# Performance work log

Measured on AMD Instinct MI355X. Metric: run time of the kernel, lower is better.

## Reference

```python
import jax, jax.numpy as jnp
import numpy as np

N = 12288
D = 128
NUM_BATCH = 32
EPS = 1e-8


def setup_inputs() -> dict:
    key = jax.random.key(0)
    kq, kk, kv, kb = jax.random.split(key, 4)
    Q = jax.random.normal(kq, (N, D), dtype=jnp.float32)
    K = jax.random.normal(kk, (N, D), dtype=jnp.float32)
    V = jax.random.normal(kv, (N, D), dtype=jnp.float32)
    batch_seg = jnp.sort(jax.random.randint(kb, (N,), 0, NUM_BATCH, dtype=jnp.int32))
    return {"Q": Q, "K": K, "V": V, "num_batch": NUM_BATCH, "batch_seg": batch_seg}


def reference(Q, K, V, num_batch, batch_seg):
    d = Q.shape[-1]
    dot = Q @ K.T                                   # [N, N]
    # NOTE: faithful to original: subtract GLOBAL max, then divide by sqrt(d)
    A = jnp.exp((dot - jnp.max(dot)) / jnp.sqrt(jnp.float32(d)))
    if num_batch > 1:
        mask = (batch_seg[None, :] == batch_seg[:, None])  # block-diagonal
        A = jnp.where(mask, A, jnp.zeros((), A.dtype))
    norm = jnp.sum(A, axis=-1, keepdims=True) + EPS
    A_weights = A / norm
    return A_weights @ V
```

## Files before the change

### kernel.cpp

```cpp
#include <hip/hip_runtime.h>


#define NN 12288
#define DD 128
#define NB 32
#define PS_LD 40

typedef __attribute__((ext_vector_type(8))) short short8;
typedef __attribute__((ext_vector_type(4))) float float4v;

__device__ __forceinline__ short f2bf(float f) {
  unsigned u = __builtin_bit_cast(unsigned, f);
  return (short)((u + 0x7FFFu + ((u >> 16) & 1u)) >> 16);
}

__device__ __forceinline__ float bf2f(short s) {
  return __builtin_bit_cast(float, ((unsigned)(unsigned short)s) << 16);
}

__device__ __forceinline__ short8 ld8_bf16(const float* p) {
  float4v f0 = *(const float4v*)p;
  float4v f1 = *(const float4v*)(p + 4);
  short8 s;
  s[0] = f2bf(f0[0]); s[1] = f2bf(f0[1]); s[2] = f2bf(f0[2]); s[3] = f2bf(f0[3]);
  s[4] = f2bf(f1[0]); s[5] = f2bf(f1[1]); s[6] = f2bf(f1[2]); s[7] = f2bf(f1[3]);
  return s;
}

__device__ __forceinline__ void dma16(const short* gsrc, short* ldst) {
  auto g = (const __attribute__((address_space(1))) void*)(unsigned long long)gsrc;
  auto l = (__attribute__((address_space(3))) void*)(unsigned)(unsigned long long)ldst;
  __builtin_amdgcn_global_load_lds(g, l, 16, 0, 0);
}

__global__ __launch_bounds__(256) void prep_kernel(
    const float* __restrict__ K, const float* __restrict__ V,
    const int* __restrict__ seg,
    short* __restrict__ Kb, short* __restrict__ Vt, int* __restrict__ starts) {
  const int tid = threadIdx.x;
  const int b = blockIdx.x;
  if (b < 768) {
    const int r0 = ((b & 7) * 96 + (b >> 3)) * 16;
    const size_t base = (size_t)r0 * DD + (size_t)tid * 8;
    *(short8*)(Kb + base) = ld8_bf16(K + base);
    const int d = tid & 127;
    const int k0 = r0 + (tid >> 7) * 8;
    short8 sv;
#pragma unroll
    for (int j = 0; j < 8; ++j) sv[j] = f2bf(V[(size_t)(k0 + j) * DD + d]);
    const int m = (k0 & 31) >> 3;
    *(short8*)(Vt + (size_t)(k0 >> 5) * 4096 + d * 32 + ((m ^ (d & 3)) * 8)) = sv;
  } else {
    int i = (b - 768) * 256 + tid;
    int s = seg[i];
    int sp = (i == 0) ? -1 : seg[i - 1];
    for (int bb = sp + 1; bb <= s; ++bb) starts[bb] = i;
    if (i == NN - 1)
      for (int bb = s + 1; bb <= NB; ++bb) starts[bb] = NN;
  }
}

__device__ __forceinline__ void issue_tile2(
    const short* __restrict__ Kb, const short* __restrict__ Vt,
    short* KshP, short* VshP, int j0, int wq, int lane) {
#pragma unroll
  for (int i = 0; i < 2; ++i) {
    const int R = wq * 8 + i * 4;
    const int row = R + (lane >> 4);
    const int dchunk = (lane & 15) ^ (row & 15);
    dma16(Kb + (size_t)(j0 + row) * DD + dchunk * 8, KshP + R * 128);
  }
  const size_t vbase = (size_t)(j0 >> 5) * 4096;
#pragma unroll
  for (int i = 0; i < 2; ++i) {
    const int off = (wq * 2 + i) * 512;
    dma16(Vt + vbase + off + lane * 8, VshP + off);
  }
}

__global__ __launch_bounds__(512, 2) void attn_fused(
    const float* __restrict__ Q, const short* __restrict__ Kb,
    const short* __restrict__ Vt, const int* __restrict__ seg,
    const int* __restrict__ starts, float* __restrict__ out) {
  __shared__ __align__(16) short Ksh[2][2][32 * 128];
  __shared__ __align__(16) short Vsh[2][2][128 * 32];
  __shared__ __align__(16) short Ps[8][16 * PS_LD];

  const int tid = threadIdx.x;
  const int w = tid >> 6;
  const int lane = tid & 63;
  const int s = w & 1;
  const int r = w >> 1;
  const int c = lane & 15;
  const int quad = lane >> 4;

  const int bid = blockIdx.x;
  const int rg = (bid & 7) * 24 + (bid >> 3);
  const int i0 = rg * 64;
  const int i0w = i0 + r * 16;

  const int L = starts[seg[i0]];
  const int H = starts[seg[i0 + 63] + 1];
  const int Lm = L & ~31;
  const int nck = (H - Lm + 31) >> 5;
  const int ck0 = s ? (nck >> 1) : 0;
  const int nt = s ? (nck - (nck >> 1)) : (nck >> 1);
  const int ntmax = nck - (nck >> 1);

  int st_r[4], en_r[4];
#pragma unroll
  for (int rr = 0; rr < 4; ++rr) {
    int sv = seg[i0w + quad * 4 + rr];
    st_r[rr] = starts[sv];
    en_r[rr] = starts[sv + 1];
  }

  short8 qf[4];
  {
    const float* qrow = Q + (size_t)(i0w + c) * DD + quad * 8;
#pragma unroll
    for (int kc = 0; kc < 4; ++kc) qf[kc] = ld8_bf16(qrow + kc * 32);
  }

  float4v acc[8];
#pragma unroll
  for (int n = 0; n < 8; ++n) acc[n] = (float4v){0.f, 0.f, 0.f, 0.f};
  float l_part[4] = {0.f, 0.f, 0.f, 0.f};

  const float scale = 0.08838834764831845f;

  if (nt > 0)
    issue_tile2(Kb, Vt, &Ksh[s][0][0], &Vsh[s][0][0], Lm + ck0 * 32, r, lane);
  __syncthreads();

  for (int t = 0; t < ntmax; ++t) {
    const int p = t & 1;
    const int j0 = Lm + (ck0 + t) * 32;
    if (t + 1 < nt)
      issue_tile2(Kb, Vt, &Ksh[s][p ^ 1][0], &Vsh[s][p ^ 1][0], j0 + 32, r, lane);

    if (t < nt) {
      float4v sa = (float4v){0.f, 0.f, 0.f, 0.f};
      float4v sb = (float4v){0.f, 0.f, 0.f, 0.f};
      const short* Kp = &Ksh[s][p][0];
#pragma unroll
      for (int kc = 0; kc < 4; ++kc) {
        const int pos = ((kc * 4 + quad) ^ c) * 8;
        short8 b0 = *(const short8*)(Kp + c * 128 + pos);
        short8 b1 = *(const short8*)(Kp + (16 + c) * 128 + pos);
        sa = __builtin_amdgcn_mfma_f32_16x16x32_bf16(qf[kc], b0, sa, 0, 0, 0);
        sb = __builtin_amdgcn_mfma_f32_16x16x32_bf16(qf[kc], b1, sb, 0, 0, 0);
      }

      const int ja = j0 + c, jb = ja + 16;
      short* prow = &Ps[w][0];
#pragma unroll
      for (int rr = 0; rr < 4; ++rr) {
        float pa = (ja >= st_r[rr] && ja < en_r[rr]) ? __expf(sa[rr] * scale) : 0.f;
        float pb = (jb >= st_r[rr] && jb < en_r[rr]) ? __expf(sb[rr] * scale) : 0.f;
        l_part[rr] += pa + pb;
        int row = quad * 4 + rr;
        prow[row * PS_LD + c]      = f2bf(pa);
        prow[row * PS_LD + 16 + c] = f2bf(pb);
      }
      short8 pf = *(const short8*)&Ps[w][c * PS_LD + quad * 8];

      const short* Vp = &Vsh[s][p][0];
      const int vpos = (quad ^ (c & 3)) * 8;
#pragma unroll
      for (int n = 0; n < 8; ++n) {
        short8 vf = *(const short8*)(Vp + (n * 16 + c) * 32 + vpos);
        acc[n] = __builtin_amdgcn_mfma_f32_16x16x32_bf16(pf, vf, acc[n], 0, 0, 0);
      }
    }

    __syncthreads();
  }

  float* Mf = reinterpret_cast<float*>(&Ksh[0][0][0]);
  float* Lf = reinterpret_cast<float*>(&Vsh[0][0][0]);
  const int ml = r * 64 + lane;
  if (s == 1) {
#pragma unroll
    for (int n = 0; n < 8; ++n)
      *(float4v*)(Mf + n * 1024 + ml * 4) = acc[n];
#pragma unroll
    for (int rr = 0; rr < 4; ++rr) Lf[rr * 256 + ml] = l_part[rr];
  }
  __syncthreads();
  if (s == 0) {
#pragma unroll
    for (int n = 0; n < 8; ++n)
      acc[n] += *(const float4v*)(Mf + n * 1024 + ml * 4);

    float inv_r[4];
#pragma unroll
    for (int rr = 0; rr < 4; ++rr) {
      float l = l_part[rr] + Lf[rr * 256 + ml];
      l += __shfl_xor(l, 1, 64);
      l += __shfl_xor(l, 2, 64);
      l += __shfl_xor(l, 4, 64);
      l += __shfl_xor(l, 8, 64);
      inv_r[rr] = 1.f / (l + 1e-8f);
    }
#pragma unroll
    for (int n = 0; n < 8; ++n)
#pragma unroll
      for (int rr = 0; rr < 4; ++rr)
        out[(size_t)(i0w + quad * 4 + rr) * DD + n * 16 + c] = acc[n][rr] * inv_r[rr];
  }
}

#define KT_LD 136
#define VT_LD 40
typedef __attribute__((ext_vector_type(4))) short short4v;

__global__ __launch_bounds__(256) void attn_fallback(
    const float* __restrict__ Q, const float* __restrict__ K,
    const float* __restrict__ V, const int* __restrict__ seg,
    float* __restrict__ out) {
  __shared__ __align__(16) short Kt[32 * KT_LD];
  __shared__ __align__(16) short Vtl[DD * VT_LD];
  __shared__ __align__(16) short Ps[4][16 * PS_LD];
  const int tid = threadIdx.x, wave = tid >> 6, lane = tid & 63;
  const int c = lane & 15, quad = lane >> 4;
  const int m0 = blockIdx.x * 64, i0 = m0 + wave * 16;
  const int segFirst = seg[m0], segLast = seg[m0 + 63];
  int lo = 0, hb = NN;
  while (lo < hb) { int mid = (lo + hb) >> 1; if (seg[mid] < segFirst) lo = mid + 1; else hb = mid; }
  int hi = lo, hb2 = NN;
  while (hi < hb2) { int mid = (hi + hb2) >> 1; if (seg[mid] <= segLast) hi = mid + 1; else hb2 = mid; }
  short8 qf[4];
  const float* qrow = Q + (size_t)(i0 + c) * DD + quad * 8;
#pragma unroll
  for (int kc = 0; kc < 4; ++kc) qf[kc] = ld8_bf16(qrow + kc * 32);
  int seg_r[4];
#pragma unroll
  for (int r = 0; r < 4; ++r) seg_r[r] = seg[i0 + quad * 4 + r];
  float4v acc[8];
#pragma unroll
  for (int n = 0; n < 8; ++n) acc[n] = (float4v){0.f, 0.f, 0.f, 0.f};
  float l_part[4] = {0.f, 0.f, 0.f, 0.f};
  const float scale = 0.08838834764831845f;
  for (int j0 = lo; j0 < hi; j0 += 32) {
    __syncthreads();
    {
      int row = tid >> 3, ch = tid & 7;
      int jj = j0 + row; if (jj > NN - 1) jj = NN - 1;
      const float* kp = K + (size_t)jj * DD + ch * 16;
      short* dst = &Kt[row * KT_LD + ch * 16];
#pragma unroll
      for (int q4 = 0; q4 < 4; ++q4) {
        float4v f = *(const float4v*)(kp + q4 * 4);
        short4v sx;
        sx[0] = f2bf(f[0]); sx[1] = f2bf(f[1]); sx[2] = f2bf(f[2]); sx[3] = f2bf(f[3]);
        *(short4v*)(dst + q4 * 4) = sx;
      }
    }
    {
      int d = tid & 127, jh = tid >> 7;
      float vv[16];
#pragma unroll
      for (int j = 0; j < 16; ++j) {
        int jj = j0 + jh * 16 + j; if (jj > NN - 1) jj = NN - 1;
        vv[j] = V[(size_t)jj * DD + d];
      }
      short8 a, b2;
#pragma unroll
      for (int j = 0; j < 8; ++j) { a[j] = f2bf(vv[j]); b2[j] = f2bf(vv[8 + j]); }
      *(short8*)&Vtl[d * VT_LD + jh * 16] = a;
      *(short8*)&Vtl[d * VT_LD + jh * 16 + 8] = b2;
    }
    __syncthreads();
    float4v sa = (float4v){0.f, 0.f, 0.f, 0.f};
    float4v sb = (float4v){0.f, 0.f, 0.f, 0.f};
    const short* krow0 = &Kt[c * KT_LD + quad * 8];
    const short* krow1 = &Kt[(16 + c) * KT_LD + quad * 8];
#pragma unroll
    for (int kc = 0; kc < 4; ++kc) {
      short8 b0 = *(const short8*)(krow0 + kc * 32);
      short8 b1 = *(const short8*)(krow1 + kc * 32);
      sa = __builtin_amdgcn_mfma_f32_16x16x32_bf16(qf[kc], b0, sa, 0, 0, 0);
      sb = __builtin_amdgcn_mfma_f32_16x16x32_bf16(qf[kc], b1, sb, 0, 0, 0);
    }
    int ja = j0 + c, jb = ja + 16;
    int sa2 = seg[ja < NN ? ja : NN - 1];
    int sb2 = seg[jb < NN ? jb : NN - 1];
    bool va = ja < hi, vb = jb < hi;
    short* prow = &Ps[wave][0];
#pragma unroll
    for (int r = 0; r < 4; ++r) {
      float pa = (va && sa2 == seg_r[r]) ? __expf(sa[r] * scale) : 0.f;
      float pb = (vb && sb2 == seg_r[r]) ? __expf(sb[r] * scale) : 0.f;
      l_part[r] += pa + pb;
      int row = quad * 4 + r;
      prow[row * PS_LD + c] = f2bf(pa);
      prow[row * PS_LD + 16 + c] = f2bf(pb);
    }
    short8 pf = *(const short8*)&Ps[wave][c * PS_LD + quad * 8];
#pragma unroll
    for (int n = 0; n < 8; ++n) {
      short8 vfr = *(const short8*)&Vtl[(n * 16 + c) * VT_LD + quad * 8];
      acc[n] = __builtin_amdgcn_mfma_f32_16x16x32_bf16(pf, vfr, acc[n], 0, 0, 0);
    }
  }
  float linv[4];
#pragma unroll
  for (int r = 0; r < 4; ++r) {
    float l = l_part[r];
    l += __shfl_xor(l, 1, 64);
    l += __shfl_xor(l, 2, 64);
    l += __shfl_xor(l, 4, 64);
    l += __shfl_xor(l, 8, 64);
    linv[r] = 1.f / (l + 1e-8f);
  }
#pragma unroll
  for (int n = 0; n < 8; ++n)
#pragma unroll
    for (int r = 0; r < 4; ++r)
      out[(size_t)(i0 + quad * 4 + r) * DD + n * 16 + c] = acc[n][r] * linv[r];
}

extern "C" void kernel_launch(void* const* d_in, const int* in_sizes, int n_in,
                              void* d_out, int out_size, void* d_ws, size_t ws_size,
                              hipStream_t stream) {
  const float* Q = (const float*)d_in[0];
  const float* K = (const float*)d_in[1];
  const float* V = (const float*)d_in[2];
  const int* seg = (const int*)d_in[4];
  float* out = (float*)d_out;

  const size_t kb_bytes = (size_t)NN * DD * sizeof(short);
  const size_t vt_bytes = (size_t)NN * DD * sizeof(short);
  const size_t st_bytes = 64 * sizeof(int);
  const size_t need = kb_bytes + vt_bytes + st_bytes;

  if (ws_size >= need) {
    char* w = (char*)d_ws;
    short* Kb = (short*)w;      w += kb_bytes;
    short* Vt = (short*)w;      w += vt_bytes;
    int* starts = (int*)w;
    prep_kernel<<<768 + NN / 256, 256, 0, stream>>>(K, V, seg, Kb, Vt, starts);
    attn_fused<<<192, 512, 0, stream>>>(Q, Kb, Vt, seg, starts, out);
  } else {
    attn_fallback<<<NN / 64, 256, 0, stream>>>(Q, K, V, seg, out);
  }
}
```

Before: 94.70 us.

## Fuse prep into single attention kernel with in-kernel segment bounds and register-staged loads

Removes the separate prep kernel that converted K/V to bf16 and computed segment starts, so a single launch does everything. Each block now finds its segment range through a windowed scan plus a binary-search fallback, and loads fp32 K/V into registers one tile ahead, converting and writing to LDS with swizzles. Masking switches to per-column segment comparison. This avoids one launch and the workspace round trip, but every block re-reads and re-converts fp32 K/V, which doubles global bytes for those tiles and replaces async LDS DMA with register staging plus an extra barrier per tile.

New measurement: 105.6 us. 1.12x slower.

```diff
diff --git a/kernel.cpp b/kernel.cpp
--- a/kernel.cpp
+++ b/kernel.cpp
@@ -3,7 +3,6 @@
 
 #define NN 12288
 #define DD 128
-#define NB 32
 #define PS_LD 40
 
 typedef __attribute__((ext_vector_type(8))) short short8;
@@ -12,10 +11,6 @@
 __device__ __forceinline__ short f2bf(float f) {
   unsigned u = __builtin_bit_cast(unsigned, f);
   return (short)((u + 0x7FFFu + ((u >> 16) & 1u)) >> 16);
-}
-
-__device__ __forceinline__ float bf2f(short s) {
-  return __builtin_bit_cast(float, ((unsigned)(unsigned short)s) << 16);
 }
 
 __device__ __forceinline__ short8 ld8_bf16(const float* p) {
@@ -27,64 +22,50 @@
   return s;
 }
 
-__device__ __forceinline__ void dma16(const short* gsrc, short* ldst) {
-  auto g = (const __attribute__((address_space(1))) void*)(unsigned long long)gsrc;
-  auto l = (__attribute__((address_space(3))) void*)(unsigned)(unsigned long long)ldst;
-  __builtin_amdgcn_global_load_lds(g, l, 16, 0, 0);
-}
-
-__global__ __launch_bounds__(256) void prep_kernel(
-    const float* __restrict__ K, const float* __restrict__ V,
-    const int* __restrict__ seg,
-    short* __restrict__ Kb, short* __restrict__ Vt, int* __restrict__ starts) {
-  const int tid = threadIdx.x;
-  const int b = blockIdx.x;
-  if (b < 768) {
-    const int r0 = ((b & 7) * 96 + (b >> 3)) * 16;
-    const size_t base = (size_t)r0 * DD + (size_t)tid * 8;
-    *(short8*)(Kb + base) = ld8_bf16(K + base);
-    const int d = tid & 127;
-    const int k0 = r0 + (tid >> 7) * 8;
-    short8 sv;
-#pragma unroll
-    for (int j = 0; j < 8; ++j) sv[j] = f2bf(V[(size_t)(k0 + j) * DD + d]);
-    const int m = (k0 & 31) >> 3;
-    *(short8*)(Vt + (size_t)(k0 >> 5) * 4096 + d * 32 + ((m ^ (d & 3)) * 8)) = sv;
-  } else {
-    int i = (b - 768) * 256 + tid;
-    int s = seg[i];
-    int sp = (i == 0) ? -1 : seg[i - 1];
-    for (int bb = sp + 1; bb <= s; ++bb) starts[bb] = i;
-    if (i == NN - 1)
-      for (int bb = s + 1; bb <= NB; ++bb) starts[bb] = NN;
-  }
-}
-
-__device__ __forceinline__ void issue_tile2(
-    const short* __restrict__ Kb, const short* __restrict__ Vt,
-    short* KshP, short* VshP, int j0, int wq, int lane) {
-#pragma unroll
-  for (int i = 0; i < 2; ++i) {
-    const int R = wq * 8 + i * 4;
-    const int row = R + (lane >> 4);
-    const int dchunk = (lane & 15) ^ (row & 15);
-    dma16(Kb + (size_t)(j0 + row) * DD + dchunk * 8, KshP + R * 128);
-  }
-  const size_t vbase = (size_t)(j0 >> 5) * 4096;
-#pragma unroll
-  for (int i = 0; i < 2; ++i) {
-    const int off = (wq * 2 + i) * 512;
-    dma16(Vt + vbase + off + lane * 8, VshP + off);
-  }
-}
-
-__global__ __launch_bounds__(512, 2) void attn_fused(
-    const float* __restrict__ Q, const short* __restrict__ Kb,
-    const short* __restrict__ Vt, const int* __restrict__ seg,
-    const int* __restrict__ starts, float* __restrict__ out) {
-  __shared__ __align__(16) short Ksh[2][2][32 * 128];
-  __shared__ __align__(16) short Vsh[2][2][128 * 32];
-  __shared__ __align__(16) short Ps[8][16 * PS_LD];
+#define SM_V 8192
+#define SM_PS 16384
+#define SM_LH 21504
+
+#define ISSUE_LOADS(J0)                                                   \
+  {                                                                       \
+    const int kr_ = min((J0) + krow, NN - 1);                             \
+    const float* kp_ = K + (size_t)kr_ * DD + kch * 16;                   \
+    kA = *(const float4v*)kp_;      kB = *(const float4v*)(kp_ + 4);      \
+    kC = *(const float4v*)(kp_ + 8); kD = *(const float4v*)(kp_ + 12);    \
+    _Pragma("unroll")                                                     \
+    for (int j_ = 0; j_ < 16; ++j_) {                                     \
+      const int vr_ = min((J0) + vkh * 16 + j_, NN - 1);                  \
+      vv[j_] = V[(size_t)vr_ * DD + vd];                                  \
+    }                                                                     \
+  }
+
+#define WRITE_LDS()                                                       \
+  {                                                                       \
+    short8 s0_, s1_;                                                      \
+    s0_[0] = f2bf(kA[0]); s0_[1] = f2bf(kA[1]);                           \
+    s0_[2] = f2bf(kA[2]); s0_[3] = f2bf(kA[3]);                           \
+    s0_[4] = f2bf(kB[0]); s0_[5] = f2bf(kB[1]);                           \
+    s0_[6] = f2bf(kB[2]); s0_[7] = f2bf(kB[3]);                           \
+    s1_[0] = f2bf(kC[0]); s1_[1] = f2bf(kC[1]);                           \
+    s1_[2] = f2bf(kC[2]); s1_[3] = f2bf(kC[3]);                           \
+    s1_[4] = f2bf(kD[0]); s1_[5] = f2bf(kD[1]);                           \
+    s1_[6] = f2bf(kD[2]); s1_[7] = f2bf(kD[3]);                           \
+    *(short8*)(KshS + krow * 128 + kwp0) = s0_;                           \
+    *(short8*)(KshS + krow * 128 + kwp1) = s1_;                           \
+    short8 v0_, v1_;                                                      \
+    _Pragma("unroll")                                                     \
+    for (int j_ = 0; j_ < 8; ++j_) {                                      \
+      v0_[j_] = f2bf(vv[j_]); v1_[j_] = f2bf(vv[8 + j_]);                 \
+    }                                                                     \
+    *(short8*)(VshS + vd * 32 + vwp0) = v0_;                              \
+    *(short8*)(VshS + vd * 32 + vwp1) = v1_;                              \
+  }
+
+__global__ __launch_bounds__(512, 2) void attn_one(
+    const float* __restrict__ Q, const float* __restrict__ K,
+    const float* __restrict__ V, const int* __restrict__ seg,
+    float* __restrict__ out) {
+  __shared__ __align__(16) short SMEM[21512];
 
   const int tid = threadIdx.x;
   const int w = tid >> 6;
@@ -93,83 +74,134 @@
   const int r = w >> 1;
   const int c = lane & 15;
   const int quad = lane >> 4;
+  const int u = r * 64 + lane;
 
   const int bid = blockIdx.x;
   const int rg = (bid & 7) * 24 + (bid >> 3);
   const int i0 = rg * 64;
   const int i0w = i0 + r * 16;
 
-  const int L = starts[seg[i0]];
-  const int H = starts[seg[i0 + 63] + 1];
+  int* LH = (int*)(SMEM + SM_LH);
+  if (tid == 0) { LH[0] = 0x7FFFFFFF; LH[1] = 0x7FFFFFFF; }
+
+  short8 qf[4];
+  {
+    const float* qrow = Q + (size_t)(i0w + c) * DD + quad * 8;
+#pragma unroll
+    for (int kc = 0; kc < 4; ++kc) qf[kc] = ld8_bf16(qrow + kc * 32);
+  }
+  int seg_r[4];
+#pragma unroll
+  for (int rr = 0; rr < 4; ++rr) seg_r[rr] = seg[i0w + quad * 4 + rr];
+  const int sFirst = seg[i0];
+  const int sLast = seg[i0 + 63];
+  __syncthreads();
+
+  {
+    int locL = 0x7FFFFFFF, locH = 0x7FFFFFFF;
+    const int ws0 = max(0, (i0 - 2040) & ~3);
+#pragma unroll
+    for (int j = 0; j < 4; ++j) {
+      int p = ws0 + tid * 4 + j;
+      if (p < NN && seg[p] >= sFirst) locL = min(locL, p);
+      int q = i0 + 64 + tid * 4 + j;
+      if (q < NN && seg[q] > sLast) locH = min(locH, q);
+    }
+#pragma unroll
+    for (int m = 1; m < 64; m <<= 1) {
+      locL = min(locL, __shfl_xor(locL, m, 64));
+      locH = min(locH, __shfl_xor(locH, m, 64));
+    }
+    if (lane == 0) {
+      atomicMin(&LH[0], locL);
+      atomicMin(&LH[1], locH);
+    }
+  }
+  __syncthreads();
+  if (tid == 0) {
+    int Lc = LH[0];
+    if (Lc > 0 && seg[Lc - 1] >= sFirst) {
+      int lo = 0, hb = Lc;
+      while (lo < hb) { int mid = (lo + hb) >> 1; if (seg[mid] < sFirst) lo = mid + 1; else hb = mid; }
+      LH[0] = lo;
+    }
+    if (LH[1] == 0x7FFFFFFF) {
+      if (i0 + 64 + 2048 >= NN) LH[1] = NN;
+      else {
+        int lo = i0 + 64, hb = NN;
+        while (lo < hb) { int mid = (lo + hb) >> 1; if (seg[mid] <= sLast) lo = mid + 1; else hb = mid; }
+        LH[1] = lo;
+      }
+    }
+  }
+  __syncthreads();
+  const int L = LH[0], H = LH[1];
+
   const int Lm = L & ~31;
   const int nck = (H - Lm + 31) >> 5;
   const int ck0 = s ? (nck >> 1) : 0;
-  const int nt = s ? (nck - (nck >> 1)) : (nck >> 1);
+  const int nt  = s ? (nck - (nck >> 1)) : (nck >> 1);
   const int ntmax = nck - (nck >> 1);
 
-  int st_r[4], en_r[4];
-#pragma unroll
-  for (int rr = 0; rr < 4; ++rr) {
-    int sv = seg[i0w + quad * 4 + rr];
-    st_r[rr] = starts[sv];
-    en_r[rr] = starts[sv + 1];
-  }
-
-  short8 qf[4];
-  {
-    const float* qrow = Q + (size_t)(i0w + c) * DD + quad * 8;
-#pragma unroll
-    for (int kc = 0; kc < 4; ++kc) qf[kc] = ld8_bf16(qrow + kc * 32);
-  }
+  const int krow = u >> 3, kch = u & 7;
+  const int vd = u & 127, vkh = u >> 7;
+  short* KshS = SMEM + s * 4096;
+  short* VshS = SMEM + SM_V + s * 4096;
+  const int kwp0 = ((2 * kch)     ^ (krow & 15)) * 8;
+  const int kwp1 = ((2 * kch + 1) ^ (krow & 15)) * 8;
+  const int vsg = (vd >> 1) & 3;
+  const int vwp0 = ((2 * vkh)     ^ vsg) * 8;
+  const int vwp1 = ((2 * vkh + 1) ^ vsg) * 8;
+
+  float4v kA, kB, kC, kD;
+  float vv[16];
 
   float4v acc[8];
 #pragma unroll
   for (int n = 0; n < 8; ++n) acc[n] = (float4v){0.f, 0.f, 0.f, 0.f};
   float l_part[4] = {0.f, 0.f, 0.f, 0.f};
-
   const float scale = 0.08838834764831845f;
 
-  if (nt > 0)
-    issue_tile2(Kb, Vt, &Ksh[s][0][0], &Vsh[s][0][0], Lm + ck0 * 32, r, lane);
-  __syncthreads();
+  if (nt > 0) ISSUE_LOADS(Lm + ck0 * 32);
 
   for (int t = 0; t < ntmax; ++t) {
-    const int p = t & 1;
     const int j0 = Lm + (ck0 + t) * 32;
-    if (t + 1 < nt)
-      issue_tile2(Kb, Vt, &Ksh[s][p ^ 1][0], &Vsh[s][p ^ 1][0], j0 + 32, r, lane);
+    if (t < nt) WRITE_LDS();
+    __syncthreads();
+    if (t + 1 < nt) ISSUE_LOADS(j0 + 32);
 
     if (t < nt) {
       float4v sa = (float4v){0.f, 0.f, 0.f, 0.f};
       float4v sb = (float4v){0.f, 0.f, 0.f, 0.f};
-      const short* Kp = &Ksh[s][p][0];
 #pragma unroll
       for (int kc = 0; kc < 4; ++kc) {
         const int pos = ((kc * 4 + quad) ^ c) * 8;
-        short8 b0 = *(const short8*)(Kp + c * 128 + pos);
-        short8 b1 = *(const short8*)(Kp + (16 + c) * 128 + pos);
+        short8 b0 = *(const short8*)(KshS + c * 128 + pos);
+        short8 b1 = *(const short8*)(KshS + (16 + c) * 128 + pos);
         sa = __builtin_amdgcn_mfma_f32_16x16x32_bf16(qf[kc], b0, sa, 0, 0, 0);
         sb = __builtin_amdgcn_mfma_f32_16x16x32_bf16(qf[kc], b1, sb, 0, 0, 0);
       }
 
       const int ja = j0 + c, jb = ja + 16;
-      short* prow = &Ps[w][0];
+      const int sa2 = seg[ja < NN ? ja : NN - 1];
+      const int sb2 = seg[jb < NN ? jb : NN - 1];
+      const bool va = ja < NN, vb = jb < NN;
+      short* prow = SMEM + SM_PS + w * (16 * PS_LD);
 #pragma unroll
       for (int rr = 0; rr < 4; ++rr) {
-        float pa = (ja >= st_r[rr] && ja < en_r[rr]) ? __expf(sa[rr] * scale) : 0.f;
-        float pb = (jb >= st_r[rr] && jb < en_r[rr]) ? __expf(sb[rr] * scale) : 0.f;
+        float pa = (va && sa2 == seg_r[rr]) ? __expf(sa[rr] * scale) : 0.f;
+        float pb = (vb && sb2 == seg_r[rr]) ? __expf(sb[rr] * scale) : 0.f;
         l_part[rr] += pa + pb;
         int row = quad * 4 + rr;
         prow[row * PS_LD + c]      = f2bf(pa);
         prow[row * PS_LD + 16 + c] = f2bf(pb);
       }
-      short8 pf = *(const short8*)&Ps[w][c * PS_LD + quad * 8];
-
-      const short* Vp = &Vsh[s][p][0];
-      const int vpos = (quad ^ (c & 3)) * 8;
+      short8 pf = *(const short8*)(prow + c * PS_LD + quad * 8);
+
+      const int vpos = (quad ^ ((c >> 1) & 3)) * 8;
 #pragma unroll
       for (int n = 0; n < 8; ++n) {
-        short8 vf = *(const short8*)(Vp + (n * 16 + c) * 32 + vpos);
+        short8 vf = *(const short8*)(VshS + (n * 16 + c) * 32 + vpos);
         acc[n] = __builtin_amdgcn_mfma_f32_16x16x32_bf16(pf, vf, acc[n], 0, 0, 0);
       }
     }
@@ -177,8 +209,8 @@
     __syncthreads();
   }
 
-  float* Mf = reinterpret_cast<float*>(&Ksh[0][0][0]);
-  float* Lf = reinterpret_cast<float*>(&Vsh[0][0][0]);
+  float* Mf = reinterpret_cast<float*>(SMEM);
+  float* Lf = reinterpret_cast<float*>(SMEM + SM_PS);
   const int ml = r * 64 + lane;
   if (s == 1) {
 #pragma unroll
@@ -209,116 +241,6 @@
       for (int rr = 0; rr < 4; ++rr)
         out[(size_t)(i0w + quad * 4 + rr) * DD + n * 16 + c] = acc[n][rr] * inv_r[rr];
   }
-}
-
-#define KT_LD 136
-#define VT_LD 40
-typedef __attribute__((ext_vector_type(4))) short short4v;
-
-__global__ __launch_bounds__(256) void attn_fallback(
-    const float* __restrict__ Q, const float* __restrict__ K,
-    const float* __restrict__ V, const int* __restrict__ seg,
-    float* __restrict__ out) {
-  __shared__ __align__(16) short Kt[32 * KT_LD];
-  __shared__ __align__(16) short Vtl[DD * VT_LD];
-  __shared__ __align__(16) short Ps[4][16 * PS_LD];
-  const int tid = threadIdx.x, wave = tid >> 6, lane = tid & 63;
-  const int c = lane & 15, quad = lane >> 4;
-  const int m0 = blockIdx.x * 64, i0 = m0 + wave * 16;
-  const int segFirst = seg[m0], segLast = seg[m0 + 63];
-  int lo = 0, hb = NN;
-  while (lo < hb) { int mid = (lo + hb) >> 1; if (seg[mid] < segFirst) lo = mid + 1; else hb = mid; }
-  int hi = lo, hb2 = NN;
-  while (hi < hb2) { int mid = (hi + hb2) >> 1; if (seg[mid] <= segLast) hi = mid + 1; else hb2 = mid; }
-  short8 qf[4];
-  const float* qrow = Q + (size_t)(i0 + c) * DD + quad * 8;
-#pragma unroll
-  for (int kc = 0; kc < 4; ++kc) qf[kc] = ld8_bf16(qrow + kc * 32);
-  int seg_r[4];
-#pragma unroll
-  for (int r = 0; r < 4; ++r) seg_r[r] = seg[i0 + quad * 4 + r];
-  float4v acc[8];
-#pragma unroll
-  for (int n = 0; n < 8; ++n) acc[n] = (float4v){0.f, 0.f, 0.f, 0.f};
-  float l_part[4] = {0.f, 0.f, 0.f, 0.f};
-  const float scale = 0.08838834764831845f;
-  for (int j0 = lo; j0 < hi; j0 += 32) {
-    __syncthreads();
-    {
-      int row = tid >> 3, ch = tid & 7;
-      int jj = j0 + row; if (jj > NN - 1) jj = NN - 1;
-      const float* kp = K + (size_t)jj * DD + ch * 16;
-      short* dst = &Kt[row * KT_LD + ch * 16];
-#pragma unroll
-      for (int q4 = 0; q4 < 4; ++q4) {
-        float4v f = *(const float4v*)(kp + q4 * 4);
-        short4v sx;
-        sx[0] = f2bf(f[0]); sx[1] = f2bf(f[1]); sx[2] = f2bf(f[2]); sx[3] = f2bf(f[3]);
-        *(short4v*)(dst + q4 * 4) = sx;
-      }
-    }
-    {
-      int d = tid & 127, jh = tid >> 7;
-      float vv[16];
-#pragma unroll
-      for (int j = 0; j < 16; ++j) {
-        int jj = j0 + jh * 16 + j; if (jj > NN - 1) jj = NN - 1;
-        vv[j] = V[(size_t)jj * DD + d];
-      }
-      short8 a, b2;
-#pragma unroll
-      for (int j = 0; j < 8; ++j) { a[j] = f2bf(vv[j]); b2[j] = f2bf(vv[8 + j]); }
-      *(short8*)&Vtl[d * VT_LD + jh * 16] = a;
-      *(short8*)&Vtl[d * VT_LD + jh * 16 + 8] = b2;
-    }
-    __syncthreads();
-    float4v sa = (float4v){0.f, 0.f, 0.f, 0.f};
-    float4v sb = (float4v){0.f, 0.f, 0.f, 0.f};
-    const short* krow0 = &Kt[c * KT_LD + quad * 8];
-    const short* krow1 = &Kt[(16 + c) * KT_LD + quad * 8];
-#pragma unroll
-    for (int kc = 0; kc < 4; ++kc) {
-      short8 b0 = *(const short8*)(krow0 + kc * 32);
-      short8 b1 = *(const short8*)(krow1 + kc * 32);
-      sa = __builtin_amdgcn_mfma_f32_16x16x32_bf16(qf[kc], b0, sa, 0, 0, 0);
-      sb = __builtin_amdgcn_mfma_f32_16x16x32_bf16(qf[kc], b1, sb, 0, 0, 0);
-    }
-    int ja = j0 + c, jb = ja + 16;
-    int sa2 = seg[ja < NN ? ja : NN - 1];
-    int sb2 = seg[jb < NN ? jb : NN - 1];
-    bool va = ja < hi, vb = jb < hi;
-    short* prow = &Ps[wave][0];
-#pragma unroll
-    for (int r = 0; r < 4; ++r) {
-      float pa = (va && sa2 == seg_r[r]) ? __expf(sa[r] * scale) : 0.f;
-      float pb = (vb && sb2 == seg_r[r]) ? __expf(sb[r] * scale) : 0.f;
-      l_part[r] += pa + pb;
-      int row = quad * 4 + r;
-      prow[row * PS_LD + c] = f2bf(pa);
-      prow[row * PS_LD + 16 + c] = f2bf(pb);
-    }
-    short8 pf = *(const short8*)&Ps[wave][c * PS_LD + quad * 8];
-#pragma unroll
-    for (int n = 0; n < 8; ++n) {
-      short8 vfr = *(const short8*)&Vtl[(n * 16 + c) * VT_LD + quad * 8];
-      acc[n] = __builtin_amdgcn_mfma_f32_16x16x32_bf16(pf, vfr, acc[n], 0, 0, 0);
-    }
-  }
-  float linv[4];
-#pragma unroll
-  for (int r = 0; r < 4; ++r) {
-    float l = l_part[r];
-    l += __shfl_xor(l, 1, 64);
-    l += __shfl_xor(l, 2, 64);
-    l += __shfl_xor(l, 4, 64);
-    l += __shfl_xor(l, 8, 64);
-    linv[r] = 1.f / (l + 1e-8f);
-  }
-#pragma unroll
-  for (int n = 0; n < 8; ++n)
-#pragma unroll
-    for (int r = 0; r < 4; ++r)
-      out[(size_t)(i0 + quad * 4 + r) * DD + n * 16 + c] = acc[n][r] * linv[r];
 }
 
 extern "C" void kernel_launch(void* const* d_in, const int* in_sizes, int n_in,
@@ -329,20 +251,7 @@
   const float* V = (const float*)d_in[2];
   const int* seg = (const int*)d_in[4];
   float* out = (float*)d_out;
-
-  const size_t kb_bytes = (size_t)NN * DD * sizeof(short);
-  const size_t vt_bytes = (size_t)NN * DD * sizeof(short);
-  const size_t st_bytes = 64 * sizeof(int);
-  const size_t need = kb_bytes + vt_bytes + st_bytes;
-
-  if (ws_size >= need) {
-    char* w = (char*)d_ws;
-    short* Kb = (short*)w;      w += kb_bytes;
-    short* Vt = (short*)w;      w += vt_bytes;
-    int* starts = (int*)w;
-    prep_kernel<<<768 + NN / 256, 256, 0, stream>>>(K, V, seg, Kb, Vt, starts);
-    attn_fused<<<192, 512, 0, stream>>>(Q, Kb, Vt, seg, starts, out);
-  } else {
-    attn_fallback<<<NN / 64, 256, 0, stream>>>(Q, K, V, seg, out);
-  }
-}
+  (void)d_ws; (void)ws_size;
+
+  attn_one<<<192, 512, 0, stream>>>(Q, K, V, seg, out);
+}
```
